# Performance work log

Hardware: AMD Instinct MI355X
Metric: run time of the kernel (lower is better)

Reference implementation:

```python
import jax, jax.numpy as jnp
import numpy as np

T, B, I, H = 512, 64, 512, 1024


def setup_inputs() -> dict:
    key = jax.random.key(0)
    ks = jax.random.split(key, 7)
    s = 0.03  # keep recurrent dynamics stable
    return {
        "X": jax.random.normal(ks[0], (T, B, I), jnp.float32),
        "h0": jax.random.normal(ks[1], (B, H), jnp.float32) * 0.1,
        "c0": jax.random.normal(ks[2], (B, H), jnp.float32) * 0.1,
        "Wi": jax.random.normal(ks[3], (4, I, H), jnp.float32) * s,
        "Wh": jax.random.normal(ks[4], (4, H, H), jnp.float32) * s,
        "bi": jnp.zeros((4, H), jnp.float32),
        "bh": jnp.zeros((4, H), jnp.float32),
    }


def reference(X, h0, c0, Wi, Wh, bi, bh):
    # Gate order along axis 0 of Wi/Wh/bi/bh: f, i, g, o (matches the torch module's
    # linear_if/hf, linear_ii/hi, linear_ig/hg, linear_io/ho pairs).
    b = bi + bh  # [4, H] combined bias, mathematically identical

    def step(carry, x_t):
        h, c = carry
        # z: [4, B, H] = x @ Wi_g + h @ Wh_g + b_g for each gate g
        z = (jnp.einsum('bi,gih->gbh', x_t, Wi)
             + jnp.einsum('bh,ghk->gbk', h, Wh)
             + b[:, None, :])
        f = jax.nn.sigmoid(z[0])
        i = jax.nn.sigmoid(z[1])
        g = jnp.tanh(z[2])
        o = jax.nn.sigmoid(z[3])
        c_new = f * c + i * g
        h_new = o * jnp.tanh(c_new)
        return (h_new, c_new), h_new

    (h_n, c_n), outputs = jax.lax.scan(step, (h0, c0), X)
    return outputs, h_n, c_n
```

## Files before the change

### kernel.cpp

```cpp
#include <hip/hip_runtime.h>
#include <stdint.h>

#define T_STEPS 512
#define NB 64
#define NI 512
#define NH 1024
#define NBLK 128

typedef __attribute__((ext_vector_type(8))) short short8;
typedef __attribute__((ext_vector_type(4))) float floatx4;
typedef __attribute__((ext_vector_type(16))) float floatx16;
typedef __attribute__((ext_vector_type(4))) unsigned short ushortx4;

__device__ __forceinline__ unsigned short f2bf(float f) {
  union { float f; uint32_t u; } v; v.f = f;
  return (unsigned short)((v.u + 0x7FFFu + ((v.u >> 16) & 1u)) >> 16);
}
__device__ __forceinline__ float bf2f(unsigned short s) {
  union { uint32_t u; float f; } v; v.u = ((uint32_t)s) << 16; return v.f;
}
__device__ __forceinline__ float sigmoid_f(float x) {
  return 1.0f / (1.0f + __expf(-x));
}
__device__ __forceinline__ float tanh_f(float x) {
  float xx = fminf(fmaxf(x, -15.0f), 15.0f);
  float e = __expf(2.0f * xx);
  return (e - 1.0f) / (e + 1.0f);
}


__global__ void convert_x(const float* __restrict__ X, unsigned short* __restrict__ Xb) {
  int i = blockIdx.x * 256 + threadIdx.x;
  floatx4 x = ((const floatx4*)X)[i];
  ushortx4 o;
  o[0] = f2bf(x[0]); o[1] = f2bf(x[1]); o[2] = f2bf(x[2]); o[3] = f2bf(x[3]);
  ((ushortx4*)Xb)[i] = o;
}

__global__ void transpose_bf16(const float* __restrict__ in, unsigned short* __restrict__ outp,
                               int K, int N) {
  __shared__ float tile[64][65];
  int g = blockIdx.z;
  int k0 = blockIdx.x * 64, n0 = blockIdx.y * 64;
  int tx = threadIdx.x & 63, ty = threadIdx.x >> 6;
  const float* src = in + (size_t)g * K * N;
  unsigned short* dst = outp + (size_t)g * K * N;
#pragma unroll
  for (int i = 0; i < 16; i++) {
    int r = ty * 16 + i;
    tile[r][tx] = src[(size_t)(k0 + r) * N + n0 + tx];
  }
  __syncthreads();
#pragma unroll
  for (int i = 0; i < 16; i++) {
    int r = ty * 16 + i;
    dst[(size_t)(n0 + r) * K + k0 + tx] = f2bf(tile[tx][r]);
  }
}

__global__ void prep_small(const float* __restrict__ bi, const float* __restrict__ bh,
                           const float* __restrict__ h0, float* __restrict__ bias,
                           unsigned short* __restrict__ hbuf0, unsigned* __restrict__ flags) {
  int i = blockIdx.x * 256 + threadIdx.x;
  if (i < NBLK) flags[i] = 0u;
  if (i < 4 * NH) bias[i] = bi[i] + bh[i];
  if (i < NB * NH) hbuf0[i] = f2bf(h0[i]);
}

__global__ __launch_bounds__(256) void gemm_zx(
    const unsigned short* __restrict__ Xb,
    const unsigned short* __restrict__ WibT,
    const float* __restrict__ bias,
    unsigned short* __restrict__ Zq) {
  __shared__ __align__(16) unsigned short As[128][40];
  __shared__ __align__(16) unsigned short Bs[128][40];
  __shared__ __align__(16) unsigned short stg[16384];
  const int g = blockIdx.z;
  const int m0 = blockIdx.x * 128;
  const int n0 = blockIdx.y * 128;
  const int tid = threadIdx.x;
  const int lane = tid & 63;
  const int wave = tid >> 6;
  const int wm = wave & 1, wn = wave >> 1;
  const int fr = lane & 15;
  const int fq = (lane >> 4) * 8;

  const unsigned short* Bsrc = WibT + (size_t)g * NH * NI;

  floatx4 acc[4][4];
#pragma unroll
  for (int a = 0; a < 4; a++)
#pragma unroll
    for (int b = 0; b < 4; b++)
#pragma unroll
      for (int z = 0; z < 4; z++) acc[a][b][z] = 0.0f;

  for (int k0 = 0; k0 < NI; k0 += 32) {
#pragma unroll
    for (int it = 0; it < 2; it++) {
      int c = tid + it * 256;
      int row = c >> 2, kc = (c & 3) * 8;
      *(uint4*)(&As[row][kc]) = *(const uint4*)(Xb + (size_t)(m0 + row) * NI + k0 + kc);
      *(uint4*)(&Bs[row][kc]) = *(const uint4*)(Bsrc + (size_t)(n0 + row) * NI + k0 + kc);
    }
    __syncthreads();
    short8 af[4], bf[4];
#pragma unroll
    for (int ms = 0; ms < 4; ms++) af[ms] = *(const short8*)(&As[wm * 64 + ms * 16 + fr][fq]);
#pragma unroll
    for (int ns = 0; ns < 4; ns++) bf[ns] = *(const short8*)(&Bs[wn * 64 + ns * 16 + fr][fq]);
#pragma unroll
    for (int ms = 0; ms < 4; ms++)
#pragma unroll
      for (int ns = 0; ns < 4; ns++)
        acc[ms][ns] = __builtin_amdgcn_mfma_f32_16x16x32_bf16(af[ms], bf[ns], acc[ms][ns], 0, 0, 0);
    __syncthreads();
  }

#pragma unroll
  for (int ns = 0; ns < 4; ns++) {
    int jrel = wn * 64 + ns * 16 + fr;
    float bs = bias[g * NH + n0 + jrel];
    int bkp = jrel >> 3, jj = jrel & 7;
#pragma unroll
    for (int ms = 0; ms < 4; ms++) {
#pragma unroll
      for (int r = 0; r < 4; r++) {
        int mrel = wm * 64 + ms * 16 + (lane >> 4) * 4 + r;
        int tp = mrel >> 6, b = mrel & 63;
        int wm2 = b >> 5, row32 = b & 31;
        int half2 = (row32 >> 2) & 1;
        int rr = (row32 & 3) | ((row32 >> 3) << 2);
        int idx = (((((tp * 16 + bkp) * 2 + wm2) * 2 + half2) * 8 + jj) * 16) + rr;
        stg[idx] = f2bf(acc[ms][ns][r] + bs);
      }
    }
  }
  __syncthreads();
  const size_t t0 = (size_t)(m0 >> 6);
  const int bk0 = n0 >> 3;
#pragma unroll
  for (int tp = 0; tp < 2; tp++) {
    size_t gbase = (((t0 + tp) * 4 + g) * 128 + bk0) * 512;
#pragma unroll
    for (int c = 0; c < 4; c++) {
      int e = c * 2048 + tid * 8;
      *(uint4*)(Zq + gbase + e) = *(const uint4*)(stg + tp * 8192 + e);
    }
  }
}


template<int G>
__device__ __forceinline__ void load_a(const unsigned short* ap, short8 (&areg)[64]) {
  asm volatile("global_load_dwordx4 %0, %1, off offset:%2 sc0 sc1"
               : "=v"(areg[G]) : "v"(ap), "i"(G * 32));
}

template<int G>
__device__ __forceinline__ void load_b(const unsigned short* bfr, int lane, short8 (&bs)[64]) {
  bs[G] = *(const short8*)(&bfr[((size_t)(G * 64) + lane) * 8]);
}

template<int G>
struct Prolog {
  static __device__ __forceinline__ void run(const unsigned short* ap, short8 (&areg)[64]) {
    load_a<G>(ap, areg);
    Prolog<G + 1>::run(ap, areg);
  }
};
template<>
struct Prolog<16> {
  static __device__ __forceinline__ void run(const unsigned short*, short8 (&)[64]) {}
};

template<int G>
struct Chunks {
  static __device__ __forceinline__ void run(const unsigned short* ap, const unsigned short* bfr,
                                             int lane, short8 (&areg)[64], short8 (&bs)[64],
                                             floatx16& acc0, floatx16& acc1) {
    if constexpr (G + 16 < 64) load_a<G + 16>(ap, areg);
    if constexpr (G + 4 < 64) load_b<G + 4>(bfr, lane, bs);
    constexpr int NOUT = (G + 16 < 64) ? 16 : (63 - G);
    asm volatile("s_waitcnt vmcnt(%1)" : "+v"(areg[G]) : "i"(NOUT) : "memory");
    if constexpr ((G & 1) == 0)
      acc0 = __builtin_amdgcn_mfma_f32_32x32x16_bf16(areg[G], bs[G], acc0, 0, 0, 0);
    else
      acc1 = __builtin_amdgcn_mfma_f32_32x32x16_bf16(areg[G], bs[G], acc1, 0, 0, 0);
    Chunks<G + 1>::run(ap, bfr, lane, areg, bs, acc0, acc1);
  }
};
template<>
struct Chunks<64> {
  static __device__ __forceinline__ void run(const unsigned short*, const unsigned short*,
                                             int, short8 (&)[64], short8 (&)[64],
                                             floatx16&, floatx16&) {}
};

__device__ __forceinline__ void lstm_step(
    int t, const unsigned short* __restrict__ Zq, unsigned short* __restrict__ hbuf,
    unsigned* __restrict__ flags, float* __restrict__ out,
    const unsigned short* bfr, const unsigned long long* fpq,
    int tid, int lane, int wm, int nl, int g0, int jj, int half, int bk, int j0,
    size_t zoff, const int (&brow)[16], float (&creg)[16],
    uint4 (&zc)[2], uint4 (&zn)[2]) {
  const int hsz = NB * NH;

  if (t) {
    unsigned tgt = (unsigned)t;
    for (;;) {
      unsigned long long fv = __hip_atomic_load(fpq, __ATOMIC_RELAXED,
                                                __HIP_MEMORY_SCOPE_AGENT);
      unsigned a = (unsigned)fv, b2 = (unsigned)(fv >> 32);
      if (__all((int)((a >= tgt) && (b2 >= tgt)))) break;
      __builtin_amdgcn_s_sleep(1);
    }
  }
  asm volatile("s_waitcnt vmcnt(0)" ::: "memory");
  __builtin_amdgcn_sched_barrier(0);

  const unsigned short* hin = hbuf + (size_t)(t & 1) * hsz;
  unsigned short* hout = hbuf + (size_t)((t + 1) & 1) * hsz;
  const unsigned short* ap = hin + (size_t)(wm * 32 + nl) * NH + half * 8;

  floatx16 acc0, acc1;
#pragma unroll
  for (int z = 0; z < 16; z++) { acc0[z] = 0.0f; acc1[z] = 0.0f; }

  short8 areg[64];
  short8 bs[64];
  Prolog<0>::run(ap, areg);
  load_b<0>(bfr, lane, bs);
  load_b<1>(bfr, lane, bs);
  load_b<2>(bfr, lane, bs);
  load_b<3>(bfr, lane, bs);
  Chunks<0>::run(ap, bfr, lane, areg, bs, acc0, acc1);
  __builtin_amdgcn_sched_barrier(0);

  if (t + 1 < T_STEPS) {
    const unsigned short* zp = Zq + (size_t)(t + 1) * 262144 + zoff;
    asm volatile("global_load_dwordx4 %0, %1, off nt" : "=v"(zn[0]) : "v"(zp));
    asm volatile("global_load_dwordx4 %0, %1, off offset:16 nt" : "=v"(zn[1]) : "v"(zp));
  }

#pragma unroll
  for (int z = 0; z < 16; z++) acc0[z] += acc1[z];

  unsigned zd[8];
  zd[0] = zc[0].x; zd[1] = zc[0].y; zd[2] = zc[0].z; zd[3] = zc[0].w;
  zd[4] = zc[1].x; zd[5] = zc[1].y; zd[6] = zc[1].z; zd[7] = zc[1].w;

  float harr[16];
#pragma unroll
  for (int r = 0; r < 16; r++) {
    unsigned dw = zd[r >> 1];
    float zxv = bf2f((unsigned short)((r & 1) ? (dw >> 16) : (dw & 0xffffu)));
    float z0 = acc0[r] + zxv;
    float z1 = __shfl_xor(z0, 8);
    float z2 = __shfl_xor(z0, 16);
    float z3 = __shfl_xor(z1, 16);
    bool bb0 = (g0 & 1) != 0, bb1 = (g0 & 2) != 0;
    float zf = bb1 ? (bb0 ? z3 : z2) : (bb0 ? z1 : z0);
    float zi = bb1 ? (bb0 ? z2 : z3) : (bb0 ? z0 : z1);
    float zg = bb1 ? (bb0 ? z1 : z0) : (bb0 ? z3 : z2);
    float zo = bb1 ? (bb0 ? z0 : z1) : (bb0 ? z2 : z3);
    float fg = sigmoid_f(zf);
    float ig = sigmoid_f(zi);
    float gg = tanh_f(zg);
    float og = sigmoid_f(zo);
    float c = fg * creg[r] + ig * gg;
    creg[r] = c;
    float h = og * tanh_f(c);
    harr[r] = h;
    if (g0 == 0) {
      __hip_atomic_store(&hout[(size_t)brow[r] * NH + j0 + jj], f2bf(h),
                         __ATOMIC_RELAXED, __HIP_MEMORY_SCOPE_AGENT);
    }
  }

  if (t + 1 < T_STEPS) {
    asm volatile("s_waitcnt vmcnt(0)" ::: "memory");
    __syncthreads();
    if (tid == 0)
      __hip_atomic_store(flags + bk, (unsigned)(t + 1),
                         __ATOMIC_RELAXED, __HIP_MEMORY_SCOPE_AGENT);
  }

  if (g0 == 0) {
#pragma unroll
    for (int r = 0; r < 16; r++) {
      size_t oidx = (size_t)brow[r] * NH + j0 + jj;
      __builtin_nontemporal_store(harr[r], &out[(size_t)t * hsz + oidx]);
      if (t == T_STEPS - 1)
        __builtin_nontemporal_store(harr[r], &out[(size_t)T_STEPS * hsz + oidx]);
    }
  }
}

__global__ __launch_bounds__(128, 1) void lstm_persist(
    const unsigned short* __restrict__ Zq,
    const unsigned short* __restrict__ WhT,
    const float* __restrict__ c0,
    unsigned short* __restrict__ hbuf,
    unsigned* __restrict__ flags,
    float* __restrict__ out) {
  __shared__ __align__(16) unsigned short bfr[64 * 64 * 8];

  const int bk = blockIdx.x;
  const int j0 = bk * 8;
  const int tid = threadIdx.x;
  const int lane = tid & 63;
  const int wm = tid >> 6;
  const int nl = lane & 31;
  const int g0 = nl >> 3;
  const int jj = nl & 7;
  const int half = lane >> 5;

  for (int i = 0; i < 32; i++) {
    int f = tid + i * 128;
    int fl = f & 63, kk = f >> 6;
    int n = fl & 31;
    size_t wrow = (size_t)((n >> 3) * NH + j0 + (n & 7));
    int kb = kk * 16 + (fl >> 5) * 8;
    uint4 v = *(const uint4*)(WhT + wrow * NH + kb);
    *(uint4*)(&bfr[(size_t)f * 8]) = v;
  }

  float creg[16];
  int brow[16];
#pragma unroll
  for (int r = 0; r < 16; r++) {
    brow[r] = wm * 32 + (r & 3) + 8 * (r >> 2) + 4 * half;
    creg[r] = c0[(size_t)brow[r] * NH + j0 + jj];
  }
  __syncthreads();

  const unsigned long long* fpq = (const unsigned long long*)flags + lane;
  const size_t zoff = (((((size_t)g0 * 128 + bk) * 2 + wm) * 2 + half) * 8 + jj) * 16;

  uint4 zA[2], zB[2];
  {
    const unsigned short* zp = Zq + zoff;
    asm volatile("global_load_dwordx4 %0, %1, off nt" : "=v"(zA[0]) : "v"(zp));
    asm volatile("global_load_dwordx4 %0, %1, off offset:16 nt" : "=v"(zA[1]) : "v"(zp));
  }

  for (int t2 = 0; t2 < T_STEPS; t2 += 2) {
    lstm_step(t2,     Zq, hbuf, flags, out, bfr, fpq, tid, lane, wm, nl, g0, jj, half,
              bk, j0, zoff, brow, creg, zA, zB);
    lstm_step(t2 + 1, Zq, hbuf, flags, out, bfr, fpq, tid, lane, wm, nl, g0, jj, half,
              bk, j0, zoff, brow, creg, zB, zA);
  }

  if (g0 == 0) {
#pragma unroll
    for (int r = 0; r < 16; r++)
      __builtin_nontemporal_store(
          creg[r], &out[(size_t)T_STEPS * NB * NH + NB * NH + (size_t)brow[r] * NH + j0 + jj]);
  }
}

extern "C" void kernel_launch(void* const* d_in, const int* in_sizes, int n_in,
                              void* d_out, int out_size, void* d_ws, size_t ws_size,
                              hipStream_t stream) {
  const float* X  = (const float*)d_in[0];
  const float* h0 = (const float*)d_in[1];
  const float* c0 = (const float*)d_in[2];
  const float* Wi = (const float*)d_in[3];
  const float* Wh = (const float*)d_in[4];
  const float* bi = (const float*)d_in[5];
  const float* bh = (const float*)d_in[6];
  float* out = (float*)d_out;

  uint8_t* ws = (uint8_t*)d_ws;
  size_t off = 0;
  auto alloc = [&](size_t bytes) -> void* {
    void* p = ws + off;
    off += (bytes + 255) & ~(size_t)255;
    return p;
  };
  unsigned short* Zq   = (unsigned short*)alloc((size_t)T_STEPS * NB * 4096 * 2);
  unsigned short* Xb   = (unsigned short*)alloc((size_t)T_STEPS * NB * NI * 2);
  unsigned short* WibT = (unsigned short*)alloc((size_t)4 * NH * NI * 2);
  unsigned short* WhT  = (unsigned short*)alloc((size_t)4 * NH * NH * 2);
  float* bias          = (float*)alloc((size_t)4 * NH * 4);
  unsigned short* hbuf = (unsigned short*)alloc((size_t)2 * NB * NH * 2);
  unsigned* flags      = (unsigned*)alloc((size_t)NBLK * 32 * 4);

  if (off > ws_size) {
    hipMemsetAsync(d_out, 0x7F, (size_t)out_size * 4, stream);
    return;
  }

  convert_x<<<16384, 256, 0, stream>>>(X, Xb);
  transpose_bf16<<<dim3(8, 16, 4), 256, 0, stream>>>(Wi, WibT, NI, NH);
  transpose_bf16<<<dim3(16, 16, 4), 256, 0, stream>>>(Wh, WhT, NH, NH);
  prep_small<<<256, 256, 0, stream>>>(bi, bh, h0, bias, hbuf, flags);
  gemm_zx<<<dim3(256, 8, 4), 256, 0, stream>>>(Xb, WibT, bias, Zq);

  lstm_persist<<<dim3(NBLK), dim3(128), 0, stream>>>(Zq, WhT, c0, hbuf, flags, out);
}
```

Measured before the change: 6.048 ms.

## Stagger h K-chunk order per block, deepen load prefetch, move Z prefetch after flag

Each block now walks the 64 K-chunks of the recurrent GEMM starting at one of four rotated offsets chosen by block index. The aim is to spread concurrent reads of the shared h buffer across different addresses instead of every block hitting the same lines together. The in-flight global load depth for h rises from 16 to 32. The next-step Z prefetch is issued after the completion flag is published, so it stays off the critical path before signalling. The cost is four template instantiations, which enlarge code size, and deeper prefetch adds register pressure.

```diff
diff --git a/kernel.cpp b/kernel.cpp
--- a/kernel.cpp
+++ b/kernel.cpp
@@ -6,6 +6,7 @@
 #define NI 512
 #define NH 1024
 #define NBLK 128
+#define DEPTH 32
 
 typedef __attribute__((ext_vector_type(8))) short short8;
 typedef __attribute__((ext_vector_type(4))) float floatx4;
@@ -151,52 +152,54 @@
 }
 
 
-template<int G>
-__device__ __forceinline__ void load_a(const unsigned short* ap, short8 (&areg)[64]) {
+template<int C>
+__device__ __forceinline__ void load_a_c(const unsigned short* ap, short8 (&areg)[64]) {
   asm volatile("global_load_dwordx4 %0, %1, off offset:%2 sc0 sc1"
-               : "=v"(areg[G]) : "v"(ap), "i"(G * 32));
-}
-
-template<int G>
-__device__ __forceinline__ void load_b(const unsigned short* bfr, int lane, short8 (&bs)[64]) {
-  bs[G] = *(const short8*)(&bfr[((size_t)(G * 64) + lane) * 8]);
-}
-
-template<int G>
-struct Prolog {
+               : "=v"(areg[C]) : "v"(ap), "i"(C * 32));
+}
+
+template<int C>
+__device__ __forceinline__ void load_b_c(const unsigned short* bfr, int lane, short8 (&bs)[64]) {
+  bs[C] = *(const short8*)(&bfr[((size_t)(C * 64) + lane) * 8]);
+}
+
+template<int S, int I>
+struct PrologR {
   static __device__ __forceinline__ void run(const unsigned short* ap, short8 (&areg)[64]) {
-    load_a<G>(ap, areg);
-    Prolog<G + 1>::run(ap, areg);
+    load_a_c<(S + I) & 63>(ap, areg);
+    PrologR<S, I + 1>::run(ap, areg);
   }
 };
-template<>
-struct Prolog<16> {
+template<int S>
+struct PrologR<S, DEPTH> {
   static __device__ __forceinline__ void run(const unsigned short*, short8 (&)[64]) {}
 };
 
-template<int G>
-struct Chunks {
+template<int S, int I>
+struct ChunksR {
   static __device__ __forceinline__ void run(const unsigned short* ap, const unsigned short* bfr,
                                              int lane, short8 (&areg)[64], short8 (&bs)[64],
                                              floatx16& acc0, floatx16& acc1) {
-    if constexpr (G + 16 < 64) load_a<G + 16>(ap, areg);
-    if constexpr (G + 4 < 64) load_b<G + 4>(bfr, lane, bs);
-    constexpr int NOUT = (G + 16 < 64) ? 16 : (63 - G);
-    asm volatile("s_waitcnt vmcnt(%1)" : "+v"(areg[G]) : "i"(NOUT) : "memory");
-    if constexpr ((G & 1) == 0)
-      acc0 = __builtin_amdgcn_mfma_f32_32x32x16_bf16(areg[G], bs[G], acc0, 0, 0, 0);
+    if constexpr (I + DEPTH < 64) load_a_c<(S + I + DEPTH) & 63>(ap, areg);
+    if constexpr (I + 4 < 64) load_b_c<(S + I + 4) & 63>(bfr, lane, bs);
+    constexpr int NOUT = (I + DEPTH < 64) ? DEPTH : (63 - I);
+    constexpr int C = (S + I) & 63;
+    asm volatile("s_waitcnt vmcnt(%1)" : "+v"(areg[C]) : "i"(NOUT) : "memory");
+    if constexpr ((I & 1) == 0)
+      acc0 = __builtin_amdgcn_mfma_f32_32x32x16_bf16(areg[C], bs[C], acc0, 0, 0, 0);
     else
-      acc1 = __builtin_amdgcn_mfma_f32_32x32x16_bf16(areg[G], bs[G], acc1, 0, 0, 0);
-    Chunks<G + 1>::run(ap, bfr, lane, areg, bs, acc0, acc1);
+      acc1 = __builtin_amdgcn_mfma_f32_32x32x16_bf16(areg[C], bs[C], acc1, 0, 0, 0);
+    ChunksR<S, I + 1>::run(ap, bfr, lane, areg, bs, acc0, acc1);
   }
 };
-template<>
-struct Chunks<64> {
+template<int S>
+struct ChunksR<S, 64> {
   static __device__ __forceinline__ void run(const unsigned short*, const unsigned short*,
                                              int, short8 (&)[64], short8 (&)[64],
                                              floatx16&, floatx16&) {}
 };
 
+template<int S>
 __device__ __forceinline__ void lstm_step(
     int t, const unsigned short* __restrict__ Zq, unsigned short* __restrict__ hbuf,
     unsigned* __restrict__ flags, float* __restrict__ out,
@@ -229,19 +232,13 @@
 
   short8 areg[64];
   short8 bs[64];
-  Prolog<0>::run(ap, areg);
-  load_b<0>(bfr, lane, bs);
-  load_b<1>(bfr, lane, bs);
-  load_b<2>(bfr, lane, bs);
-  load_b<3>(bfr, lane, bs);
-  Chunks<0>::run(ap, bfr, lane, areg, bs, acc0, acc1);
+  PrologR<S, 0>::run(ap, areg);
+  load_b_c<(S + 0) & 63>(bfr, lane, bs);
+  load_b_c<(S + 1) & 63>(bfr, lane, bs);
+  load_b_c<(S + 2) & 63>(bfr, lane, bs);
+  load_b_c<(S + 3) & 63>(bfr, lane, bs);
+  ChunksR<S, 0>::run(ap, bfr, lane, areg, bs, acc0, acc1);
   __builtin_amdgcn_sched_barrier(0);
-
-  if (t + 1 < T_STEPS) {
-    const unsigned short* zp = Zq + (size_t)(t + 1) * 262144 + zoff;
-    asm volatile("global_load_dwordx4 %0, %1, off nt" : "=v"(zn[0]) : "v"(zp));
-    asm volatile("global_load_dwordx4 %0, %1, off offset:16 nt" : "=v"(zn[1]) : "v"(zp));
-  }
 
 #pragma unroll
   for (int z = 0; z < 16; z++) acc0[z] += acc1[z];
@@ -284,6 +281,9 @@
     if (tid == 0)
       __hip_atomic_store(flags + bk, (unsigned)(t + 1),
                          __ATOMIC_RELAXED, __HIP_MEMORY_SCOPE_AGENT);
+    const unsigned short* zp = Zq + (size_t)(t + 1) * 262144 + zoff;
+    asm volatile("global_load_dwordx4 %0, %1, off nt" : "=v"(zn[0]) : "v"(zp));
+    asm volatile("global_load_dwordx4 %0, %1, off offset:16 nt" : "=v"(zn[1]) : "v"(zp));
   }
 
   if (g0 == 0) {
@@ -294,6 +294,27 @@
       if (t == T_STEPS - 1)
         __builtin_nontemporal_store(harr[r], &out[(size_t)T_STEPS * hsz + oidx]);
     }
+  }
+}
+
+template<int S>
+__device__ __forceinline__ void lstm_loop(
+    const unsigned short* __restrict__ Zq, unsigned short* __restrict__ hbuf,
+    unsigned* __restrict__ flags, float* __restrict__ out,
+    const unsigned short* bfr, const unsigned long long* fpq,
+    int tid, int lane, int wm, int nl, int g0, int jj, int half, int bk, int j0,
+    size_t zoff, const int (&brow)[16], float (&creg)[16]) {
+  uint4 zA[2], zB[2];
+  {
+    const unsigned short* zp = Zq + zoff;
+    asm volatile("global_load_dwordx4 %0, %1, off nt" : "=v"(zA[0]) : "v"(zp));
+    asm volatile("global_load_dwordx4 %0, %1, off offset:16 nt" : "=v"(zA[1]) : "v"(zp));
+  }
+  for (int t2 = 0; t2 < T_STEPS; t2 += 2) {
+    lstm_step<S>(t2,     Zq, hbuf, flags, out, bfr, fpq, tid, lane, wm, nl, g0, jj,
+                 half, bk, j0, zoff, brow, creg, zA, zB);
+    lstm_step<S>(t2 + 1, Zq, hbuf, flags, out, bfr, fpq, tid, lane, wm, nl, g0, jj,
+                 half, bk, j0, zoff, brow, creg, zB, zA);
   }
 }
 
@@ -338,18 +359,15 @@
   const unsigned long long* fpq = (const unsigned long long*)flags + lane;
   const size_t zoff = (((((size_t)g0 * 128 + bk) * 2 + wm) * 2 + half) * 8 + jj) * 16;
 
-  uint4 zA[2], zB[2];
-  {
-    const unsigned short* zp = Zq + zoff;
-    asm volatile("global_load_dwordx4 %0, %1, off nt" : "=v"(zA[0]) : "v"(zp));
-    asm volatile("global_load_dwordx4 %0, %1, off offset:16 nt" : "=v"(zA[1]) : "v"(zp));
-  }
-
-  for (int t2 = 0; t2 < T_STEPS; t2 += 2) {
-    lstm_step(t2,     Zq, hbuf, flags, out, bfr, fpq, tid, lane, wm, nl, g0, jj, half,
-              bk, j0, zoff, brow, creg, zA, zB);
-    lstm_step(t2 + 1, Zq, hbuf, flags, out, bfr, fpq, tid, lane, wm, nl, g0, jj, half,
-              bk, j0, zoff, brow, creg, zB, zA);
+  switch (bk & 3) {
+    case 0: lstm_loop<0>(Zq, hbuf, flags, out, bfr, fpq, tid, lane, wm, nl, g0, jj,
+                         half, bk, j0, zoff, brow, creg); break;
+    case 1: lstm_loop<16>(Zq, hbuf, flags, out, bfr, fpq, tid, lane, wm, nl, g0, jj,
+                          half, bk, j0, zoff, brow, creg); break;
+    case 2: lstm_loop<32>(Zq, hbuf, flags, out, bfr, fpq, tid, lane, wm, nl, g0, jj,
+                          half, bk, j0, zoff, brow, creg); break;
+    default: lstm_loop<48>(Zq, hbuf, flags, out, bfr, fpq, tid, lane, wm, nl, g0, jj,
+                           half, bk, j0, zoff, brow, creg); break;
   }
 
   if (g0 == 0) {
```

Measured after the change: 5.881 ms. 1.03x faster.
